# Performance work log

Hardware: AMD Instinct MI355X
Metric: run time of the kernel (lower is better)

The kernel has to match this reference:

```python
import jax, jax.numpy as jnp
import numpy as np

N, E, DIN, DH, H, B = 50000, 800000, 128, 32, 8, 512
NEG_SLOPE = 0.2


def glorot(key, shape):
    fan_in, fan_out = shape[0], shape[-1]
    lim = (6.0 / (fan_in + fan_out)) ** 0.5
    return jax.random.uniform(key, shape, jnp.float32, -lim, lim)


def setup_inputs() -> dict:
    key = jax.random.key(0)
    ks = jax.random.split(key, 16)
    x = jax.random.normal(ks[0], (N, DIN), jnp.float32)
    edge_index = jax.random.randint(ks[1], (2, E), 0, N, jnp.int64)
    batch = jnp.sort(jax.random.randint(ks[2], (N,), 0, B, jnp.int64))
    edge_weight = jax.random.uniform(ks[3], (E, 1), jnp.float32)
    # layer 1: GATv2Conv(DIN -> DH, heads=H, edge_dim=1)
    Wl1 = glorot(ks[4], (DIN, H * DH))
    Wr1 = glorot(ks[5], (DIN, H * DH))
    We1 = glorot(ks[6], (1, H * DH))
    att1 = glorot(ks[7], (H, DH))
    b1 = jnp.zeros((H * DH,), jnp.float32)
    # layer 2: GATv2Conv(H*DH -> DH, heads=1, edge_dim=1)
    Wl2 = glorot(ks[8], (H * DH, DH))
    Wr2 = glorot(ks[9], (H * DH, DH))
    We2 = glorot(ks[10], (1, DH))
    att2 = glorot(ks[11], (1, DH))
    b2 = jnp.zeros((DH,), jnp.float32)
    Wfc = glorot(ks[12], (DH, 1))
    bfc = jnp.zeros((1,), jnp.float32)
    return dict(x=x, edge_index=edge_index, batch=batch, edge_weight=edge_weight,
                Wl1=Wl1, Wr1=Wr1, We1=We1, att1=att1, b1=b1,
                Wl2=Wl2, Wr2=Wr2, We2=We2, att2=att2, b2=b2,
                Wfc=Wfc, bfc=bfc)


def gatv2_layer(x, src, dst, ew, Wl, Wr, We, att, bias, heads, out_ch):
    n = x.shape[0]
    xl = (x @ Wl).reshape(n, heads, out_ch)   # source transform
    xr = (x @ Wr).reshape(n, heads, out_ch)   # target transform
    ee = (ew @ We).reshape(-1, heads, out_ch)  # edge attr transform
    z = xl[src] + xr[dst] + ee                 # [E,H,C]
    s = jnp.einsum('ehc,hc->eh', jax.nn.leaky_relu(z, NEG_SLOPE), att)
    # segment softmax over edges sharing the same target node
    m = jax.ops.segment_max(s, dst, num_segments=n)
    ex = jnp.exp(s - m[dst])
    den = jax.ops.segment_sum(ex, dst, num_segments=n)
    alpha = ex / (den[dst] + 1e-16)            # [E,H]
    out = jax.ops.segment_sum(alpha[..., None] * xl[src], dst, num_segments=n)
    return out.reshape(n, heads * out_ch) + bias


def add_self_loops(edge_index, edge_weight, n):
    loops = jnp.arange(n, dtype=edge_index.dtype)
    src = jnp.concatenate([edge_index[0], loops])
    dst = jnp.concatenate([edge_index[1], loops])
    fill = jnp.mean(edge_weight, axis=0, keepdims=True)  # fill_value='mean'
    ew = jnp.concatenate([edge_weight, jnp.broadcast_to(fill, (n, edge_weight.shape[1]))])
    return src, dst, ew


def reference(x, edge_index, batch, edge_weight,
              Wl1, Wr1, We1, att1, b1,
              Wl2, Wr2, We2, att2, b2,
              Wfc, bfc):
    n = x.shape[0]
    src, dst, ew = add_self_loops(edge_index, edge_weight, n)
    h = gatv2_layer(x, src, dst, ew, Wl1, Wr1, We1, att1, b1, H, DH)
    h = jax.nn.relu(h)
    h = gatv2_layer(h, src, dst, ew, Wl2, Wr2, We2, att2, b2, 1, DH)
    feat = jax.nn.relu(h)
    # global mean pool over graphs
    sums = jax.ops.segment_sum(feat, batch, num_segments=B)
    cnt = jax.ops.segment_sum(jnp.ones((n, 1), feat.dtype), batch, num_segments=B)
    feat = sums / jnp.maximum(cnt, 1.0)
    feat = jax.nn.sigmoid(feat)
    return feat @ Wfc + bfc  # [B,1]
```

## Files before the change

### kernel.cpp

```cpp
#include <hip/hip_runtime.h>
#include <math.h>

#define N_NODES 50000
#define N_EDGES 800000
#define D_IN    128
#define D_H     32
#define N_HEADS 8
#define N_GRAPHS 512
#define E_TOT   (N_EDGES + N_NODES)
#define HDIM    (N_HEADS * D_H)
#define NEG_SLOPE 0.2f
#define NSCAN_BLK ((N_NODES + 255) / 256)
#define LOG2E 1.4426950408889634f
#define RESCALE_THR2 11.0f

typedef short bfrag8 __attribute__((ext_vector_type(8)));
typedef float f32x4 __attribute__((ext_vector_type(4)));
typedef float f32x2 __attribute__((ext_vector_type(2)));

#if __has_builtin(__builtin_amdgcn_exp2f)
#define EXP2(x) __builtin_amdgcn_exp2f(x)
#else
#define EXP2(x) exp2f(x)
#endif

__device__ __forceinline__ unsigned short f2b(float x) {
    unsigned u = __float_as_uint(x);
    unsigned r = u + 0x7FFFu + ((u >> 16) & 1u);
    return (unsigned short)(r >> 16);
}
__device__ __forceinline__ f32x2 b2x2(unsigned u) {
    f32x2 v;
    v.x = __uint_as_float(u << 16);
    v.y = __uint_as_float(u & 0xFFFF0000u);
    return v;
}

__device__ __forceinline__ float dpp8_sum(float x) {
    x += __int_as_float(__builtin_amdgcn_mov_dpp(__float_as_int(x), 0xB1, 0xF, 0xF, true));
    x += __int_as_float(__builtin_amdgcn_mov_dpp(__float_as_int(x), 0x4E, 0xF, 0xF, true));
    x += __int_as_float(__builtin_amdgcn_mov_dpp(__float_as_int(x), 0x141, 0xF, 0xF, true));
    return x;
}

#define RS_BLK   512
#define HIST_BLK ((E_TOT + 255) / 256)
#define W1_BLK   (512 * 128 / 256)
#define W2_BLK   (64 * 256 / 256)
__global__ void k_front(const float* __restrict__ ew, const int* __restrict__ ei,
                        const float* __restrict__ Wl1, const float* __restrict__ Wr1,
                        const float* __restrict__ Wl2, const float* __restrict__ Wr2,
                        float* __restrict__ fillsum, int* __restrict__ deg,
                        unsigned short* __restrict__ Wt1,
                        unsigned short* __restrict__ Wt2) {
    __shared__ float ls[4];
    int b = blockIdx.x;
    if (b < RS_BLK) {
        int t = b * 256 + threadIdx.x;
        float s = 0.f;
        for (int i = t; i < N_EDGES; i += RS_BLK * 256) s += ew[i];
        for (int m = 1; m < 64; m <<= 1) s += __shfl_xor(s, m);
        int lane = threadIdx.x & 63, wv = threadIdx.x >> 6;
        if (lane == 0) ls[wv] = s;
        __syncthreads();
        if (threadIdx.x == 0) atomicAdd(fillsum, ls[0] + ls[1] + ls[2] + ls[3]);
    } else if (b < RS_BLK + HIST_BLK) {
        int e = (b - RS_BLK) * 256 + threadIdx.x;
        if (e >= E_TOT) return;
        int dst = (e < N_EDGES) ? ei[N_EDGES + e] : (e - N_EDGES);
        atomicAdd(&deg[dst], 1);
    } else if (b < RS_BLK + HIST_BLK + W1_BLK) {
        int t = (b - RS_BLK - HIST_BLK) * 256 + threadIdx.x;
        int c = t >> 7, k = t & 127;
        float v = (c < 256) ? Wl1[k * 256 + c] : Wr1[k * 256 + (c - 256)];
        Wt1[t] = f2b(v);
    } else {
        int t = (b - RS_BLK - HIST_BLK - W1_BLK) * 256 + threadIdx.x;
        int c = t >> 8, k = t & 255;
        float v = (c < 32) ? Wl2[k * 32 + c] : Wr2[k * 32 + (c - 32)];
        Wt2[t] = f2b(v);
    }
}

__global__ void k_scan1(const int* __restrict__ deg, int* __restrict__ start,
                        int* __restrict__ bsum) {
    __shared__ int sh[256];
    int i = blockIdx.x * 256 + threadIdx.x;
    int v = (i < N_NODES) ? deg[i] : 0;
    sh[threadIdx.x] = v;
    __syncthreads();
    for (int o = 1; o < 256; o <<= 1) {
        int t = (threadIdx.x >= o) ? sh[threadIdx.x - o] : 0;
        __syncthreads();
        sh[threadIdx.x] += t;
        __syncthreads();
    }
    if (i < N_NODES) start[i] = sh[threadIdx.x] - v;
    if (threadIdx.x == 255) bsum[blockIdx.x] = sh[255];
}
__global__ void k_scan2(int* __restrict__ bsum, int nb) {
    __shared__ int sh[256];
    int v = (threadIdx.x < nb) ? bsum[threadIdx.x] : 0;
    sh[threadIdx.x] = v;
    __syncthreads();
    for (int o = 1; o < 256; o <<= 1) {
        int t = (threadIdx.x >= o) ? sh[threadIdx.x - o] : 0;
        __syncthreads();
        sh[threadIdx.x] += t;
        __syncthreads();
    }
    if (threadIdx.x < nb) bsum[threadIdx.x] = sh[threadIdx.x] - v;
}
__global__ void k_scan3(int* __restrict__ start, const int* __restrict__ bsum,
                        int* __restrict__ cur) {
    int i = blockIdx.x * 256 + threadIdx.x;
    if (i < N_NODES) {
        int v = start[i] + bsum[blockIdx.x];
        start[i] = v;
        cur[i] = v;
    }
}

__global__ void k_scatter(const int* __restrict__ ei, const float* __restrict__ ew,
                          const float* __restrict__ fillsum,
                          int* __restrict__ cur, int2* __restrict__ csr) {
    int e = blockIdx.x * blockDim.x + threadIdx.x;
    if (e >= E_TOT) return;
    int src, dst; float w;
    if (e < N_EDGES) { src = ei[e]; dst = ei[N_EDGES + e]; w = ew[e]; }
    else { src = dst = e - N_EDGES; w = fillsum[0] * (1.0f / N_EDGES); }
    int pos = atomicAdd(&cur[dst], 1);
    csr[pos] = make_int2(src, __float_as_int(w));
}

template <int KC, bool F32A>
__global__ __launch_bounds__(256) void k_gemm_bf16(
    const void* __restrict__ Av, const unsigned short* __restrict__ Bt,
    unsigned short* __restrict__ C, int M, int N)
{
    __shared__ unsigned short A_lds[64][KC + 8];
    __shared__ unsigned short B_lds[64][KC + 8];
    int row0 = blockIdx.y * 64, col0 = blockIdx.x * 64;
    int tid = threadIdx.x;
    if constexpr (F32A) {
        const float* A = (const float*)Av;
        const int C4 = KC / 4;
        for (int idx = tid; idx < 64 * C4; idx += 256) {
            int r = idx / C4, c4 = idx % C4;
            int gr = row0 + r;
            float4 v = {0.f, 0.f, 0.f, 0.f};
            if (gr < M) v = ((const float4*)(A + (size_t)gr * KC))[c4];
            ushort4 o;
            o.x = f2b(v.x); o.y = f2b(v.y); o.z = f2b(v.z); o.w = f2b(v.w);
            *(ushort4*)&A_lds[r][c4 * 4] = o;
        }
    } else {
        const unsigned short* A = (const unsigned short*)Av;
        const int CPR = KC / 8;
        for (int idx = tid; idx < 64 * CPR; idx += 256) {
            int r = idx / CPR, ch = idx % CPR;
            int gr = row0 + r;
            uint4 v = {0u, 0u, 0u, 0u};
            if (gr < M) v = *(const uint4*)(A + (size_t)gr * KC + ch * 8);
            *(uint4*)&A_lds[r][ch * 8] = v;
        }
    }
    {
        const int CPR = KC / 8;
        for (int idx = tid; idx < 64 * CPR; idx += 256) {
            int r = idx / CPR, ch = idx % CPR;
            uint4 v = *(const uint4*)(Bt + (size_t)(col0 + r) * KC + ch * 8);
            *(uint4*)&B_lds[r][ch * 8] = v;
        }
    }
    __syncthreads();

    int wid = tid >> 6, lane = tid & 63;
    int wy = wid >> 1, wx = wid & 1;
    int lr = lane & 15, lh = lane >> 4;
    f32x4 acc[2][2] = {};
    #pragma unroll
    for (int k0 = 0; k0 < KC; k0 += 32) {
        bfrag8 a0 = *(const bfrag8*)&A_lds[32 * wy + lr][k0 + lh * 8];
        bfrag8 a1 = *(const bfrag8*)&A_lds[32 * wy + 16 + lr][k0 + lh * 8];
        bfrag8 b0 = *(const bfrag8*)&B_lds[32 * wx + lr][k0 + lh * 8];
        bfrag8 b1 = *(const bfrag8*)&B_lds[32 * wx + 16 + lr][k0 + lh * 8];
        acc[0][0] = __builtin_amdgcn_mfma_f32_16x16x32_bf16(a0, b0, acc[0][0], 0, 0, 0);
        acc[0][1] = __builtin_amdgcn_mfma_f32_16x16x32_bf16(a0, b1, acc[0][1], 0, 0, 0);
        acc[1][0] = __builtin_amdgcn_mfma_f32_16x16x32_bf16(a1, b0, acc[1][0], 0, 0, 0);
        acc[1][1] = __builtin_amdgcn_mfma_f32_16x16x32_bf16(a1, b1, acc[1][1], 0, 0, 0);
    }
    #pragma unroll
    for (int mt = 0; mt < 2; ++mt) {
        #pragma unroll
        for (int nt = 0; nt < 2; ++nt) {
            #pragma unroll
            for (int r = 0; r < 4; ++r) {
                int row = row0 + 32 * wy + 16 * mt + lh * 4 + r;
                if (row < M)
                    C[(size_t)row * N + col0 + 32 * wx + 16 * nt + lr] = f2b(acc[mt][nt][r]);
            }
        }
    }
}

__global__ __launch_bounds__(256) void k_gat1(
    const unsigned short* __restrict__ xlr,
    const int* __restrict__ start, const int* __restrict__ deg,
    const int2* __restrict__ csr,
    const float* __restrict__ We, const float* __restrict__ att,
    const float* __restrict__ b1, unsigned short* __restrict__ out1)
{
    int wid = (blockIdx.x * blockDim.x + threadIdx.x) >> 6;
    int lane = threadIdx.x & 63;
    if (wid >= N_NODES) return;
    f32x2 we01 = ((const f32x2*)We)[2 * lane],  we23 = ((const f32x2*)We)[2 * lane + 1];
    f32x2 at01 = ((const f32x2*)att)[2 * lane], at23 = ((const f32x2*)att)[2 * lane + 1];
    at01 *= LOG2E; at23 *= LOG2E;
    uint2 xru = *(const uint2*)(xlr + (size_t)wid * 512 + 256 + 4 * lane);
    f32x2 xr01 = b2x2(xru.x), xr23 = b2x2(xru.y);
    int s0 = start[wid], dg = deg[wid];
    const int2* ep = csr + s0;
    float m = -1e30f, d = 0.f;
    f32x2 acc01 = {0.f, 0.f}, acc23 = {0.f, 0.f};

    int dmax = dg - 1;
    int2 e0 = ep[0];
    int2 e1 = ep[1 < dmax ? 1 : dmax];
    int2 e2 = ep[2 < dmax ? 2 : dmax];
    int2 e3 = ep[3 < dmax ? 3 : dmax];
    uint2 r0 = *(const uint2*)(xlr + ((size_t)e0.x << 9) + 4 * lane);
    uint2 r1 = *(const uint2*)(xlr + ((size_t)e1.x << 9) + 4 * lane);
    uint2 r2 = *(const uint2*)(xlr + ((size_t)e2.x << 9) + 4 * lane);
    uint2 r3 = *(const uint2*)(xlr + ((size_t)e3.x << 9) + 4 * lane);

    for (int j = 0; j < dg; j += 4) {
        float w0 = __int_as_float(e0.y), w1 = __int_as_float(e1.y);
        float w2 = __int_as_float(e2.y), w3 = __int_as_float(e3.y);
        f32x2 a001 = b2x2(r0.x), a023 = b2x2(r0.y);
        f32x2 a101 = b2x2(r1.x), a123 = b2x2(r1.y);
        f32x2 a201 = b2x2(r2.x), a223 = b2x2(r2.y);
        f32x2 a301 = b2x2(r3.x), a323 = b2x2(r3.y);
        int jn = j + 4;
        if (jn < dg) {
            e0 = ep[jn];
            e1 = ep[jn + 1 < dmax ? jn + 1 : dmax];
            e2 = ep[jn + 2 < dmax ? jn + 2 : dmax];
            e3 = ep[jn + 3 < dmax ? jn + 3 : dmax];
            r0 = *(const uint2*)(xlr + ((size_t)e0.x << 9) + 4 * lane);
            r1 = *(const uint2*)(xlr + ((size_t)e1.x << 9) + 4 * lane);
            r2 = *(const uint2*)(xlr + ((size_t)e2.x << 9) + 4 * lane);
            r3 = *(const uint2*)(xlr + ((size_t)e3.x << 9) + 4 * lane);
        }
        f32x2 z, lz;
        f32x2 ww, pv;
        ww = (f32x2){w0, w0}; pv = (f32x2){0.f, 0.f};
        z = a001 + __builtin_elementwise_fma(ww, we01, xr01);
        lz = __builtin_elementwise_max(z, z * NEG_SLOPE);
        pv = __builtin_elementwise_fma(lz, at01, pv);
        z = a023 + __builtin_elementwise_fma(ww, we23, xr23);
        lz = __builtin_elementwise_max(z, z * NEG_SLOPE);
        pv = __builtin_elementwise_fma(lz, at23, pv);
        float p0 = pv.x + pv.y;
        ww = (f32x2){w1, w1}; pv = (f32x2){0.f, 0.f};
        z = a101 + __builtin_elementwise_fma(ww, we01, xr01);
        lz = __builtin_elementwise_max(z, z * NEG_SLOPE);
        pv = __builtin_elementwise_fma(lz, at01, pv);
        z = a123 + __builtin_elementwise_fma(ww, we23, xr23);
        lz = __builtin_elementwise_max(z, z * NEG_SLOPE);
        pv = __builtin_elementwise_fma(lz, at23, pv);
        float p1 = pv.x + pv.y;
        ww = (f32x2){w2, w2}; pv = (f32x2){0.f, 0.f};
        z = a201 + __builtin_elementwise_fma(ww, we01, xr01);
        lz = __builtin_elementwise_max(z, z * NEG_SLOPE);
        pv = __builtin_elementwise_fma(lz, at01, pv);
        z = a223 + __builtin_elementwise_fma(ww, we23, xr23);
        lz = __builtin_elementwise_max(z, z * NEG_SLOPE);
        pv = __builtin_elementwise_fma(lz, at23, pv);
        float p2 = pv.x + pv.y;
        ww = (f32x2){w3, w3}; pv = (f32x2){0.f, 0.f};
        z = a301 + __builtin_elementwise_fma(ww, we01, xr01);
        lz = __builtin_elementwise_max(z, z * NEG_SLOPE);
        pv = __builtin_elementwise_fma(lz, at01, pv);
        z = a323 + __builtin_elementwise_fma(ww, we23, xr23);
        lz = __builtin_elementwise_max(z, z * NEG_SLOPE);
        pv = __builtin_elementwise_fma(lz, at23, pv);
        float p3 = pv.x + pv.y;
        p0 = dpp8_sum(p0); p1 = dpp8_sum(p1);
        p2 = dpp8_sum(p2); p3 = dpp8_sum(p3);
        if (j + 1 >= dg) p1 = -1e30f;
        if (j + 2 >= dg) p2 = -1e30f;
        if (j + 3 >= dg) p3 = -1e30f;
        float pm = fmaxf(fmaxf(p0, p1), fmaxf(p2, p3));
        if (__any(pm > m + RESCALE_THR2)) {
            float nm = fmaxf(m, pm);
            float sc = EXP2(m - nm);
            d *= sc;
            acc01 *= sc; acc23 *= sc;
            m = nm;
        }
        float q0 = EXP2(p0 - m), q1 = EXP2(p1 - m);
        float q2 = EXP2(p2 - m), q3 = EXP2(p3 - m);
        d += (q0 + q1) + (q2 + q3);
        f32x2 qq;
        qq = (f32x2){q0, q0};
        acc01 = __builtin_elementwise_fma(qq, a001, acc01);
        acc23 = __builtin_elementwise_fma(qq, a023, acc23);
        qq = (f32x2){q1, q1};
        acc01 = __builtin_elementwise_fma(qq, a101, acc01);
        acc23 = __builtin_elementwise_fma(qq, a123, acc23);
        qq = (f32x2){q2, q2};
        acc01 = __builtin_elementwise_fma(qq, a201, acc01);
        acc23 = __builtin_elementwise_fma(qq, a223, acc23);
        qq = (f32x2){q3, q3};
        acc01 = __builtin_elementwise_fma(qq, a301, acc01);
        acc23 = __builtin_elementwise_fma(qq, a323, acc23);
    }
    float inv = 1.f / (d + 1e-16f);
    f32x2 b01 = ((const f32x2*)b1)[2 * lane], b23 = ((const f32x2*)b1)[2 * lane + 1];
    ushort4 o;
    o.x = f2b(fmaxf(fmaf(acc01.x, inv, b01.x), 0.f));
    o.y = f2b(fmaxf(fmaf(acc01.y, inv, b01.y), 0.f));
    o.z = f2b(fmaxf(fmaf(acc23.x, inv, b23.x), 0.f));
    o.w = f2b(fmaxf(fmaf(acc23.y, inv, b23.y), 0.f));
    *(ushort4*)(out1 + (size_t)wid * 256 + 4 * lane) = o;
}

__global__ __launch_bounds__(256) void k_gat2(
    const unsigned short* __restrict__ xlr2,
    const int* __restrict__ start, const int* __restrict__ deg,
    const int2* __restrict__ csr,
    const float* __restrict__ We, const float* __restrict__ att,
    const float* __restrict__ b2, const int* __restrict__ batch,
    float* __restrict__ pool, float* __restrict__ cnt)
{
    int gt = blockIdx.x * blockDim.x + threadIdx.x;
    int i = gt >> 3, g = gt & 7;
    if (i >= N_NODES) return;
    f32x2 we01 = ((const f32x2*)We)[2 * g],  we23 = ((const f32x2*)We)[2 * g + 1];
    f32x2 at01 = ((const f32x2*)att)[2 * g], at23 = ((const f32x2*)att)[2 * g + 1];
    at01 *= LOG2E; at23 *= LOG2E;
    uint2 xru = *(const uint2*)(xlr2 + (size_t)i * 64 + 32 + 4 * g);
    f32x2 xr01 = b2x2(xru.x), xr23 = b2x2(xru.y);
    int s0 = start[i], dg = deg[i];
    const int2* ep = csr + s0;
    float m = -1e30f, d = 0.f;
    f32x2 acc01 = {0.f, 0.f}, acc23 = {0.f, 0.f};

    int2 ec0 = ep[0];
    int2 ec1 = ep[dg > 1 ? 1 : 0];
    uint2 ra0 = *(const uint2*)(xlr2 + ((size_t)ec0.x << 6) + 4 * g);
    uint2 ra1 = *(const uint2*)(xlr2 + ((size_t)ec1.x << 6) + 4 * g);

    for (int j = 0; j < dg; j += 2) {
        int2 c0 = ec0, c1 = ec1;
        uint2 A0 = ra0, A1 = ra1;
        int jn = j + 2;
        if (jn < dg) {
            ec0 = ep[jn];
            ec1 = ep[(jn + 1 < dg) ? jn + 1 : jn];
            ra0 = *(const uint2*)(xlr2 + ((size_t)ec0.x << 6) + 4 * g);
            ra1 = *(const uint2*)(xlr2 + ((size_t)ec1.x << 6) + 4 * g);
        }
        float w0 = __int_as_float(c0.y), w1 = __int_as_float(c1.y);
        f32x2 ww0 = {w0, w0}, ww1 = {w1, w1};
        f32x2 a001 = b2x2(A0.x), a023 = b2x2(A0.y);
        f32x2 a101 = b2x2(A1.x), a123 = b2x2(A1.y);
        f32x2 p0v = {0.f, 0.f}, p1v = {0.f, 0.f}, z, lz;
        z = a001 + __builtin_elementwise_fma(ww0, we01, xr01);
        lz = __builtin_elementwise_max(z, z * NEG_SLOPE);
        p0v = __builtin_elementwise_fma(lz, at01, p0v);
        z = a023 + __builtin_elementwise_fma(ww0, we23, xr23);
        lz = __builtin_elementwise_max(z, z * NEG_SLOPE);
        p0v = __builtin_elementwise_fma(lz, at23, p0v);
        z = a101 + __builtin_elementwise_fma(ww1, we01, xr01);
        lz = __builtin_elementwise_max(z, z * NEG_SLOPE);
        p1v = __builtin_elementwise_fma(lz, at01, p1v);
        z = a123 + __builtin_elementwise_fma(ww1, we23, xr23);
        lz = __builtin_elementwise_max(z, z * NEG_SLOPE);
        p1v = __builtin_elementwise_fma(lz, at23, p1v);
        float p0 = dpp8_sum(p0v.x + p0v.y);
        float p1 = dpp8_sum(p1v.x + p1v.y);
        if (j + 1 >= dg) p1 = -1e30f;
        float pm = fmaxf(p0, p1);
        if (__any(pm > m + RESCALE_THR2)) {
            float nm = fmaxf(m, pm);
            float sc = EXP2(m - nm);
            d *= sc;
            acc01 *= sc; acc23 *= sc;
            m = nm;
        }
        float q0 = EXP2(p0 - m), q1 = EXP2(p1 - m);
        d += q0 + q1;
        f32x2 qq0 = {q0, q0}, qq1 = {q1, q1};
        acc01 = __builtin_elementwise_fma(qq0, a001, acc01);
        acc23 = __builtin_elementwise_fma(qq0, a023, acc23);
        acc01 = __builtin_elementwise_fma(qq1, a101, acc01);
        acc23 = __builtin_elementwise_fma(qq1, a123, acc23);
    }
    float inv = 1.f / (d + 1e-16f);
    f32x2 b01 = ((const f32x2*)b2)[2 * g], b23 = ((const f32x2*)b2)[2 * g + 1];
    float vx = fmaxf(fmaf(acc01.x, inv, b01.x), 0.f);
    float vy = fmaxf(fmaf(acc01.y, inv, b01.y), 0.f);
    float vz = fmaxf(fmaf(acc23.x, inv, b23.x), 0.f);
    float vw = fmaxf(fmaf(acc23.y, inv, b23.y), 0.f);
    int b = batch[i];
    float* o = pool + (size_t)b * D_H + g * 4;
    atomicAdd(o + 0, vx);
    atomicAdd(o + 1, vy);
    atomicAdd(o + 2, vz);
    atomicAdd(o + 3, vw);
    if (g == 0) atomicAdd(&cnt[b], 1.0f);
}

__global__ void k_final(const float* __restrict__ pool, const float* __restrict__ cnt,
                        const float* __restrict__ Wfc, const float* __restrict__ bfc,
                        float* __restrict__ out)
{
    int b = blockIdx.x * blockDim.x + threadIdx.x;
    if (b >= N_GRAPHS) return;
    float c = cnt[b]; c = c > 1.f ? c : 1.f;
    float acc = 0.f;
    #pragma unroll
    for (int j = 0; j < D_H; ++j) {
        float f = pool[b * D_H + j] / c;
        f = 1.f / (1.f + __expf(-f));
        acc = fmaf(f, Wfc[j], acc);
    }
    out[b] = acc + bfc[0];
}

extern "C" void kernel_launch(void* const* d_in, const int* in_sizes, int n_in,
                              void* d_out, int out_size, void* d_ws, size_t ws_size,
                              hipStream_t stream)
{
    const float* x    = (const float*)d_in[0];
    const int*   ei   = (const int*)  d_in[1];
    const int*   batch= (const int*)  d_in[2];
    const float* ew   = (const float*)d_in[3];
    const float* Wl1  = (const float*)d_in[4];
    const float* Wr1  = (const float*)d_in[5];
    const float* We1  = (const float*)d_in[6];
    const float* att1 = (const float*)d_in[7];
    const float* b1   = (const float*)d_in[8];
    const float* Wl2  = (const float*)d_in[9];
    const float* Wr2  = (const float*)d_in[10];
    const float* We2  = (const float*)d_in[11];
    const float* att2 = (const float*)d_in[12];
    const float* b2   = (const float*)d_in[13];
    const float* Wfc  = (const float*)d_in[14];
    const float* bfc  = (const float*)d_in[15];
    float* out = (float*)d_out;

    float* ws = (float*)d_ws;
    size_t off = 0;
    auto take = [&](size_t n) -> float* {
        float* p = ws + off;
        off = (off + n + 63) & ~(size_t)63;
        return p;
    };
    float* fillsum = take(1);
    int*   deg  = (int*)take(N_NODES);
    float* cnt  = take(N_GRAPHS);
    float* pool = take((size_t)N_GRAPHS * D_H);
    size_t zero_elems = off;
    int*   start = (int*)take(N_NODES);
    int*   cur   = (int*)take(N_NODES);
    int*   bsum  = (int*)take(256);
    int2*  csr   = (int2*)take((size_t)E_TOT * 2);
    unsigned short* Wt1  = (unsigned short*)take(512 * 128 / 2);
    unsigned short* Wt2  = (unsigned short*)take(64 * 256 / 2);
    unsigned short* xlr1 = (unsigned short*)take((size_t)N_NODES * 512 / 2);
    unsigned short* out1 = (unsigned short*)take((size_t)N_NODES * 256 / 2);
    unsigned short* xlr2 = (unsigned short*)take((size_t)N_NODES * 64 / 2);
    (void)ws_size; (void)in_sizes; (void)n_in; (void)out_size;

    hipMemsetAsync(d_ws, 0, zero_elems * sizeof(float), stream);

    k_front<<<RS_BLK + HIST_BLK + W1_BLK + W2_BLK, 256, 0, stream>>>(
        ew, ei, Wl1, Wr1, Wl2, Wr2, fillsum, deg, Wt1, Wt2);

    k_scan1<<<NSCAN_BLK, 256, 0, stream>>>(deg, start, bsum);
    k_scan2<<<1, 256, 0, stream>>>(bsum, NSCAN_BLK);
    k_scan3<<<NSCAN_BLK, 256, 0, stream>>>(start, bsum, cur);
    k_scatter<<<(E_TOT + 255) / 256, 256, 0, stream>>>(ei, ew, fillsum, cur, csr);

    k_gemm_bf16<128, true><<<dim3(512 / 64, (N_NODES + 63) / 64), 256, 0, stream>>>(
        x, Wt1, xlr1, N_NODES, 512);

    k_gat1<<<(N_NODES * 64 + 255) / 256, 256, 0, stream>>>(
        xlr1, start, deg, csr, We1, att1, b1, out1);

    k_gemm_bf16<256, false><<<dim3(64 / 64, (N_NODES + 63) / 64), 256, 0, stream>>>(
        out1, Wt2, xlr2, N_NODES, 64);

    k_gat2<<<((size_t)N_NODES * 8 + 255) / 256, 256, 0, stream>>>(
        xlr2, start, deg, csr, We2, att2, b2, batch, pool, cnt);

    k_final<<<(N_GRAPHS + 255) / 256, 256, 0, stream>>>(pool, cnt, Wfc, bfc, out);
}
```

Before: 330.1 us.

## Enlarge layer-1 GEMM tiles to 128x128 and unroll layer-2 edge loop by four

The first projection GEMM now uses 128x128 block tiles, with each wave computing a 64x64 sub-tile of 16 MFMA accumulators. This cuts how often the fp32 x rows are re-read and converted across column blocks, at the cost of more LDS and registers per block and fewer blocks. The layer-2 attention kernel now processes four edges per iteration instead of two, so more gathers are in flight to hide gather latency, in exchange for higher register use. The second GEMM is specialised into its own kernel with no change to its algorithm.

Result: no change. 334.7 us (+1.4%).

```diff
diff --git a/kernel.cpp b/kernel.cpp
--- a/kernel.cpp
+++ b/kernel.cpp
@@ -133,45 +133,84 @@
     csr[pos] = make_int2(src, __float_as_int(w));
 }
 
-template <int KC, bool F32A>
-__global__ __launch_bounds__(256) void k_gemm_bf16(
-    const void* __restrict__ Av, const unsigned short* __restrict__ Bt,
-    unsigned short* __restrict__ C, int M, int N)
+__global__ __launch_bounds__(256) void k_gemm1(
+    const float* __restrict__ A, const unsigned short* __restrict__ Bt,
+    unsigned short* __restrict__ C, int M)
 {
+    const int KC = 128, NN = 512;
+    __shared__ unsigned short A_lds[128][KC + 8];
+    __shared__ unsigned short B_lds[128][KC + 8];
+    int row0 = blockIdx.y * 128, col0 = blockIdx.x * 128;
+    int tid = threadIdx.x;
+    for (int idx = tid; idx < 128 * 32; idx += 256) {
+        int r = idx >> 5, c4 = idx & 31;
+        int gr = row0 + r;
+        float4 v = {0.f, 0.f, 0.f, 0.f};
+        if (gr < M) v = ((const float4*)(A + (size_t)gr * KC))[c4];
+        ushort4 o;
+        o.x = f2b(v.x); o.y = f2b(v.y); o.z = f2b(v.z); o.w = f2b(v.w);
+        *(ushort4*)&A_lds[r][c4 * 4] = o;
+    }
+    for (int idx = tid; idx < 128 * 16; idx += 256) {
+        int r = idx >> 4, ch = idx & 15;
+        uint4 v = *(const uint4*)(Bt + (size_t)(col0 + r) * KC + ch * 8);
+        *(uint4*)&B_lds[r][ch * 8] = v;
+    }
+    __syncthreads();
+
+    int wid = tid >> 6, lane = tid & 63;
+    int wy = wid >> 1, wx = wid & 1;
+    int lr = lane & 15, lh = lane >> 4;
+    f32x4 acc[4][4] = {};
+    #pragma unroll
+    for (int k0 = 0; k0 < KC; k0 += 32) {
+        bfrag8 af[4], bf[4];
+        #pragma unroll
+        for (int i = 0; i < 4; ++i) {
+            af[i] = *(const bfrag8*)&A_lds[64 * wy + 16 * i + lr][k0 + lh * 8];
+            bf[i] = *(const bfrag8*)&B_lds[64 * wx + 16 * i + lr][k0 + lh * 8];
+        }
+        #pragma unroll
+        for (int mi = 0; mi < 4; ++mi)
+            #pragma unroll
+            for (int ni = 0; ni < 4; ++ni)
+                acc[mi][ni] = __builtin_amdgcn_mfma_f32_16x16x32_bf16(af[mi], bf[ni], acc[mi][ni], 0, 0, 0);
+    }
+    #pragma unroll
+    for (int mi = 0; mi < 4; ++mi) {
+        #pragma unroll
+        for (int ni = 0; ni < 4; ++ni) {
+            #pragma unroll
+            for (int r = 0; r < 4; ++r) {
+                int row = row0 + 64 * wy + 16 * mi + lh * 4 + r;
+                if (row < M)
+                    C[(size_t)row * NN + col0 + 64 * wx + 16 * ni + lr] = f2b(acc[mi][ni][r]);
+            }
+        }
+    }
+}
+
+__global__ __launch_bounds__(256) void k_gemm2(
+    const unsigned short* __restrict__ A, const unsigned short* __restrict__ Bt,
+    unsigned short* __restrict__ C, int M)
+{
+    const int KC = 256, NN = 64;
     __shared__ unsigned short A_lds[64][KC + 8];
     __shared__ unsigned short B_lds[64][KC + 8];
-    int row0 = blockIdx.y * 64, col0 = blockIdx.x * 64;
+    int row0 = blockIdx.y * 64, col0 = 0;
     int tid = threadIdx.x;
-    if constexpr (F32A) {
-        const float* A = (const float*)Av;
-        const int C4 = KC / 4;
-        for (int idx = tid; idx < 64 * C4; idx += 256) {
-            int r = idx / C4, c4 = idx % C4;
-            int gr = row0 + r;
-            float4 v = {0.f, 0.f, 0.f, 0.f};
-            if (gr < M) v = ((const float4*)(A + (size_t)gr * KC))[c4];
-            ushort4 o;
-            o.x = f2b(v.x); o.y = f2b(v.y); o.z = f2b(v.z); o.w = f2b(v.w);
-            *(ushort4*)&A_lds[r][c4 * 4] = o;
-        }
-    } else {
-        const unsigned short* A = (const unsigned short*)Av;
-        const int CPR = KC / 8;
-        for (int idx = tid; idx < 64 * CPR; idx += 256) {
-            int r = idx / CPR, ch = idx % CPR;
-            int gr = row0 + r;
-            uint4 v = {0u, 0u, 0u, 0u};
-            if (gr < M) v = *(const uint4*)(A + (size_t)gr * KC + ch * 8);
-            *(uint4*)&A_lds[r][ch * 8] = v;
-        }
-    }
-    {
-        const int CPR = KC / 8;
-        for (int idx = tid; idx < 64 * CPR; idx += 256) {
-            int r = idx / CPR, ch = idx % CPR;
-            uint4 v = *(const uint4*)(Bt + (size_t)(col0 + r) * KC + ch * 8);
-            *(uint4*)&B_lds[r][ch * 8] = v;
-        }
+    const int CPR = KC / 8;
+    for (int idx = tid; idx < 64 * CPR; idx += 256) {
+        int r = idx / CPR, ch = idx % CPR;
+        int gr = row0 + r;
+        uint4 v = {0u, 0u, 0u, 0u};
+        if (gr < M) v = *(const uint4*)(A + (size_t)gr * KC + ch * 8);
+        *(uint4*)&A_lds[r][ch * 8] = v;
+    }
+    for (int idx = tid; idx < 64 * CPR; idx += 256) {
+        int r = idx / CPR, ch = idx % CPR;
+        uint4 v = *(const uint4*)(Bt + (size_t)(col0 + r) * KC + ch * 8);
+        *(uint4*)&B_lds[r][ch * 8] = v;
     }
     __syncthreads();
 
@@ -198,7 +237,7 @@
             for (int r = 0; r < 4; ++r) {
                 int row = row0 + 32 * wy + 16 * mt + lh * 4 + r;
                 if (row < M)
-                    C[(size_t)row * N + col0 + 32 * wx + 16 * nt + lr] = f2b(acc[mt][nt][r]);
+                    C[(size_t)row * NN + col0 + 32 * wx + 16 * nt + lr] = f2b(acc[mt][nt][r]);
             }
         }
     }
@@ -252,8 +291,7 @@
             r2 = *(const uint2*)(xlr + ((size_t)e2.x << 9) + 4 * lane);
             r3 = *(const uint2*)(xlr + ((size_t)e3.x << 9) + 4 * lane);
         }
-        f32x2 z, lz;
-        f32x2 ww, pv;
+        f32x2 z, lz, ww, pv;
         ww = (f32x2){w0, w0}; pv = (f32x2){0.f, 0.f};
         z = a001 + __builtin_elementwise_fma(ww, we01, xr01);
         lz = __builtin_elementwise_max(z, z * NEG_SLOPE);
@@ -347,42 +385,73 @@
     float m = -1e30f, d = 0.f;
     f32x2 acc01 = {0.f, 0.f}, acc23 = {0.f, 0.f};
 
-    int2 ec0 = ep[0];
-    int2 ec1 = ep[dg > 1 ? 1 : 0];
-    uint2 ra0 = *(const uint2*)(xlr2 + ((size_t)ec0.x << 6) + 4 * g);
-    uint2 ra1 = *(const uint2*)(xlr2 + ((size_t)ec1.x << 6) + 4 * g);
-
-    for (int j = 0; j < dg; j += 2) {
-        int2 c0 = ec0, c1 = ec1;
-        uint2 A0 = ra0, A1 = ra1;
-        int jn = j + 2;
+    int dmax = dg - 1;
+    int2 e0 = ep[0];
+    int2 e1 = ep[1 < dmax ? 1 : dmax];
+    int2 e2 = ep[2 < dmax ? 2 : dmax];
+    int2 e3 = ep[3 < dmax ? 3 : dmax];
+    uint2 r0 = *(const uint2*)(xlr2 + ((size_t)e0.x << 6) + 4 * g);
+    uint2 r1 = *(const uint2*)(xlr2 + ((size_t)e1.x << 6) + 4 * g);
+    uint2 r2 = *(const uint2*)(xlr2 + ((size_t)e2.x << 6) + 4 * g);
+    uint2 r3 = *(const uint2*)(xlr2 + ((size_t)e3.x << 6) + 4 * g);
+
+    for (int j = 0; j < dg; j += 4) {
+        float w0 = __int_as_float(e0.y), w1 = __int_as_float(e1.y);
+        float w2 = __int_as_float(e2.y), w3 = __int_as_float(e3.y);
+        f32x2 a001 = b2x2(r0.x), a023 = b2x2(r0.y);
+        f32x2 a101 = b2x2(r1.x), a123 = b2x2(r1.y);
+        f32x2 a201 = b2x2(r2.x), a223 = b2x2(r2.y);
+        f32x2 a301 = b2x2(r3.x), a323 = b2x2(r3.y);
+        int jn = j + 4;
         if (jn < dg) {
-            ec0 = ep[jn];
-            ec1 = ep[(jn + 1 < dg) ? jn + 1 : jn];
-            ra0 = *(const uint2*)(xlr2 + ((size_t)ec0.x << 6) + 4 * g);
-            ra1 = *(const uint2*)(xlr2 + ((size_t)ec1.x << 6) + 4 * g);
-        }
-        float w0 = __int_as_float(c0.y), w1 = __int_as_float(c1.y);
-        f32x2 ww0 = {w0, w0}, ww1 = {w1, w1};
-        f32x2 a001 = b2x2(A0.x), a023 = b2x2(A0.y);
-        f32x2 a101 = b2x2(A1.x), a123 = b2x2(A1.y);
-        f32x2 p0v = {0.f, 0.f}, p1v = {0.f, 0.f}, z, lz;
-        z = a001 + __builtin_elementwise_fma(ww0, we01, xr01);
-        lz = __builtin_elementwise_max(z, z * NEG_SLOPE);
-        p0v = __builtin_elementwise_fma(lz, at01, p0v);
-        z = a023 + __builtin_elementwise_fma(ww0, we23, xr23);
-        lz = __builtin_elementwise_max(z, z * NEG_SLOPE);
-        p0v = __builtin_elementwise_fma(lz, at23, p0v);
-        z = a101 + __builtin_elementwise_fma(ww1, we01, xr01);
-        lz = __builtin_elementwise_max(z, z * NEG_SLOPE);
-        p1v = __builtin_elementwise_fma(lz, at01, p1v);
-        z = a123 + __builtin_elementwise_fma(ww1, we23, xr23);
-        lz = __builtin_elementwise_max(z, z * NEG_SLOPE);
-        p1v = __builtin_elementwise_fma(lz, at23, p1v);
-        float p0 = dpp8_sum(p0v.x + p0v.y);
-        float p1 = dpp8_sum(p1v.x + p1v.y);
+            e0 = ep[jn];
+            e1 = ep[jn + 1 < dmax ? jn + 1 : dmax];
+            e2 = ep[jn + 2 < dmax ? jn + 2 : dmax];
+            e3 = ep[jn + 3 < dmax ? jn + 3 : dmax];
+            r0 = *(const uint2*)(xlr2 + ((size_t)e0.x << 6) + 4 * g);
+            r1 = *(const uint2*)(xlr2 + ((size_t)e1.x << 6) + 4 * g);
+            r2 = *(const uint2*)(xlr2 + ((size_t)e2.x << 6) + 4 * g);
+            r3 = *(const uint2*)(xlr2 + ((size_t)e3.x << 6) + 4 * g);
+        }
+        f32x2 z, lz, ww, pv;
+        ww = (f32x2){w0, w0}; pv = (f32x2){0.f, 0.f};
+        z = a001 + __builtin_elementwise_fma(ww, we01, xr01);
+        lz = __builtin_elementwise_max(z, z * NEG_SLOPE);
+        pv = __builtin_elementwise_fma(lz, at01, pv);
+        z = a023 + __builtin_elementwise_fma(ww, we23, xr23);
+        lz = __builtin_elementwise_max(z, z * NEG_SLOPE);
+        pv = __builtin_elementwise_fma(lz, at23, pv);
+        float p0 = pv.x + pv.y;
+        ww = (f32x2){w1, w1}; pv = (f32x2){0.f, 0.f};
+        z = a101 + __builtin_elementwise_fma(ww, we01, xr01);
+        lz = __builtin_elementwise_max(z, z * NEG_SLOPE);
+        pv = __builtin_elementwise_fma(lz, at01, pv);
+        z = a123 + __builtin_elementwise_fma(ww, we23, xr23);
+        lz = __builtin_elementwise_max(z, z * NEG_SLOPE);
+        pv = __builtin_elementwise_fma(lz, at23, pv);
+        float p1 = pv.x + pv.y;
+        ww = (f32x2){w2, w2}; pv = (f32x2){0.f, 0.f};
+        z = a201 + __builtin_elementwise_fma(ww, we01, xr01);
+        lz = __builtin_elementwise_max(z, z * NEG_SLOPE);
+        pv = __builtin_elementwise_fma(lz, at01, pv);
+        z = a223 + __builtin_elementwise_fma(ww, we23, xr23);
+        lz = __builtin_elementwise_max(z, z * NEG_SLOPE);
+        pv = __builtin_elementwise_fma(lz, at23, pv);
+        float p2 = pv.x + pv.y;
+        ww = (f32x2){w3, w3}; pv = (f32x2){0.f, 0.f};
+        z = a301 + __builtin_elementwise_fma(ww, we01, xr01);
+        lz = __builtin_elementwise_max(z, z * NEG_SLOPE);
+        pv = __builtin_elementwise_fma(lz, at01, pv);
+        z = a323 + __builtin_elementwise_fma(ww, we23, xr23);
+        lz = __builtin_elementwise_max(z, z * NEG_SLOPE);
+        pv = __builtin_elementwise_fma(lz, at23, pv);
+        float p3 = pv.x + pv.y;
+        p0 = dpp8_sum(p0); p1 = dpp8_sum(p1);
+        p2 = dpp8_sum(p2); p3 = dpp8_sum(p3);
         if (j + 1 >= dg) p1 = -1e30f;
-        float pm = fmaxf(p0, p1);
+        if (j + 2 >= dg) p2 = -1e30f;
+        if (j + 3 >= dg) p3 = -1e30f;
+        float pm = fmaxf(fmaxf(p0, p1), fmaxf(p2, p3));
         if (__any(pm > m + RESCALE_THR2)) {
             float nm = fmaxf(m, pm);
             float sc = EXP2(m - nm);
@@ -391,12 +460,21 @@
             m = nm;
         }
         float q0 = EXP2(p0 - m), q1 = EXP2(p1 - m);
-        d += q0 + q1;
-        f32x2 qq0 = {q0, q0}, qq1 = {q1, q1};
-        acc01 = __builtin_elementwise_fma(qq0, a001, acc01);
-        acc23 = __builtin_elementwise_fma(qq0, a023, acc23);
-        acc01 = __builtin_elementwise_fma(qq1, a101, acc01);
-        acc23 = __builtin_elementwise_fma(qq1, a123, acc23);
+        float q2 = EXP2(p2 - m), q3 = EXP2(p3 - m);
+        d += (q0 + q1) + (q2 + q3);
+        f32x2 qq;
+        qq = (f32x2){q0, q0};
+        acc01 = __builtin_elementwise_fma(qq, a001, acc01);
+        acc23 = __builtin_elementwise_fma(qq, a023, acc23);
+        qq = (f32x2){q1, q1};
+        acc01 = __builtin_elementwise_fma(qq, a101, acc01);
+        acc23 = __builtin_elementwise_fma(qq, a123, acc23);
+        qq = (f32x2){q2, q2};
+        acc01 = __builtin_elementwise_fma(qq, a201, acc01);
+        acc23 = __builtin_elementwise_fma(qq, a223, acc23);
+        qq = (f32x2){q3, q3};
+        acc01 = __builtin_elementwise_fma(qq, a301, acc01);
+        acc23 = __builtin_elementwise_fma(qq, a323, acc23);
     }
     float inv = 1.f / (d + 1e-16f);
     f32x2 b01 = ((const f32x2*)b2)[2 * g], b23 = ((const f32x2*)b2)[2 * g + 1];
@@ -485,14 +563,14 @@
     k_scan3<<<NSCAN_BLK, 256, 0, stream>>>(start, bsum, cur);
     k_scatter<<<(E_TOT + 255) / 256, 256, 0, stream>>>(ei, ew, fillsum, cur, csr);
 
-    k_gemm_bf16<128, true><<<dim3(512 / 64, (N_NODES + 63) / 64), 256, 0, stream>>>(
-        x, Wt1, xlr1, N_NODES, 512);
+    k_gemm1<<<dim3(512 / 128, (N_NODES + 127) / 128), 256, 0, stream>>>(
+        x, Wt1, xlr1, N_NODES);
 
     k_gat1<<<(N_NODES * 64 + 255) / 256, 256, 0, stream>>>(
         xlr1, start, deg, csr, We1, att1, b1, out1);
 
-    k_gemm_bf16<256, false><<<dim3(64 / 64, (N_NODES + 63) / 64), 256, 0, stream>>>(
-        out1, Wt2, xlr2, N_NODES, 64);
+    k_gemm2<<<dim3(1, (N_NODES + 63) / 64), 256, 0, stream>>>(
+        out1, Wt2, xlr2, N_NODES);
 
     k_gat2<<<((size_t)N_NODES * 8 + 255) / 256, 256, 0, stream>>>(
         xlr2, start, deg, csr, We2, att2, b2, batch, pool, cnt);
```
